# Performance work log

Hardware: AMD Instinct MI355X
Metric: run time of the kernel (lower is better)

## Reference

```python
import jax, jax.numpy as jnp
import numpy as np

B = 512
N_DRUGS = 4096
H_DRUG = 1023          # per-drug feature dim; input to MLP is 2*(H_DRUG+1) = 2048
N_CELL = 32
DIMS = [2048, 2048, 1024, 512, 1]


def setup_inputs() -> dict:
    key = jax.random.key(0)
    ks = jax.random.split(key, 12)
    pairs = jax.random.randint(ks[0], (B, 2), 0, N_DRUGS)
    cell_lines = jax.random.randint(ks[1], (B,), 0, N_CELL)
    attrs = jax.random.normal(ks[2], (B, 4), dtype=jnp.float32)
    h_drug = jax.random.normal(ks[3], (N_DRUGS, H_DRUG), dtype=jnp.float32)
    # shared Linear layers (torch Linear: y = x @ W.T + b), kaiming-uniform-ish init
    def lin(k, fan_in, fan_out):
        k1, k2 = jax.random.split(k)
        bound = 1.0 / np.sqrt(fan_in)
        W = jax.random.uniform(k1, (fan_out, fan_in), jnp.float32, -bound, bound)
        b = jax.random.uniform(k2, (fan_out,), jnp.float32, -bound, bound)
        return W, b
    W0, b0 = lin(ks[4], DIMS[0], DIMS[1])
    W1, b1 = lin(ks[5], DIMS[1], DIMS[2])
    # cell-line specific layers: 1/100 * randn
    L0 = 0.01 * jax.random.normal(ks[6], (N_CELL, DIMS[3], DIMS[2]), dtype=jnp.float32)
    O0 = 0.01 * jax.random.normal(ks[7], (N_CELL, DIMS[3], 1), dtype=jnp.float32)
    L1 = 0.01 * jax.random.normal(ks[8], (N_CELL, DIMS[4], DIMS[3]), dtype=jnp.float32)
    O1 = 0.01 * jax.random.normal(ks[9], (N_CELL, DIMS[4], 1), dtype=jnp.float32)
    return {"pairs": pairs, "cell_lines": cell_lines, "attrs": attrs, "h_drug": h_drug,
            "W0": W0, "b0": b0, "W1": W1, "b1": b1,
            "L0": L0, "O0": O0, "L1": L1, "O1": O1}


def reference(pairs, cell_lines, attrs, h_drug, W0, b0, W1, b1, L0, O0, L1, O1):
    n_attr = attrs.shape[1] // 2
    h1 = h_drug[pairs[:, 0]]                               # [B, H_DRUG]
    h2 = h_drug[pairs[:, 1]]
    bd1 = jnp.concatenate([h1, attrs[:, n_attr - 1:n_attr]], axis=1)
    bd2 = jnp.concatenate([h2, attrs[:, -1:]], axis=1)
    # original flips order with p=0.5 (data augmentation); fixed to (bd1, bd2) for determinism
    x = jnp.concatenate([bd1, bd2], axis=1)                # [B, 2048]
    # shared MLP (note: original applies relu(relu(x)) == relu(x))
    x = jax.nn.relu(x @ W0.T + b0)                         # [B, 2048]
    x = jax.nn.relu(x @ W1.T + b1)                         # [B, 1024]
    # cell-line-specific layers: gather per-sample weight and batched matvec
    x = jax.nn.relu(jnp.einsum('boi,bi->bo', L0[cell_lines], x) + O0[cell_lines, :, 0])  # [B, 512]
    x = jnp.einsum('boi,bi->bo', L1[cell_lines], x) + O1[cell_lines, :, 0]               # [B, 1]
    return x[:, 0]
```

## Files before the change

kernel.cpp:

```cpp
#include <hip/hip_runtime.h>

typedef short s16x8 __attribute__((ext_vector_type(8)));
typedef float f32x4 __attribute__((ext_vector_type(4)));
typedef unsigned short u16;

#define BATCH 512
#define HD    1023
#define K0    2048
#define N0    2048
#define N1    1024
#define N2    512

__device__ __forceinline__ u16 f2bf(float f) {
  unsigned u = __builtin_bit_cast(unsigned, f);
  unsigned r = (u + 0x7fffu + ((u >> 16) & 1u)) >> 16;
  return (u16)r;
}

__device__ __forceinline__ s16x8 pack8(f32x4 a, f32x4 b) {
  s16x8 r;
  r[0] = (short)f2bf(a[0]); r[1] = (short)f2bf(a[1]);
  r[2] = (short)f2bf(a[2]); r[3] = (short)f2bf(a[3]);
  r[4] = (short)f2bf(b[0]); r[5] = (short)f2bf(b[1]);
  r[6] = (short)f2bf(b[2]); r[7] = (short)f2bf(b[3]);
  return r;
}

__global__ __launch_bounds__(256) void k_gather(const int* __restrict__ pairs,
    const float* __restrict__ attrs, const float* __restrict__ h_drug,
    u16* __restrict__ xb) {
  int b = blockIdx.x;
  const float* h0 = h_drug + (size_t)pairs[2 * b] * HD;
  const float* h1 = h_drug + (size_t)pairs[2 * b + 1] * HD;
  u16* xr = xb + (size_t)b * K0;
  for (int i = threadIdx.x; i < HD; i += 256) {
    xr[i] = f2bf(h0[i]);
    xr[1024 + i] = f2bf(h1[i]);
  }
  if (threadIdx.x == 0) {
    xr[1023] = f2bf(attrs[4 * b + 1]);
    xr[2047] = f2bf(attrs[4 * b + 3]);
  }
}

#define GI(s, t) { \
  const size_t ab = (size_t)(t) * 128; const int wf = (t) * 64; \
  pa0_##s = *(const s16x8*)(agp0 + ab); \
  if constexpr (AF == 2) pa1_##s = *(const s16x8*)(agp1 + ab); \
  pw0_##s = *(const f32x4*)(wgp + wf); pw1_##s = *(const f32x4*)(wgp + wf + 4); }

#define GS(s, t, DOLOAD) { \
  char* buf = lds[(s) & 1]; \
  *(s16x8*)(buf + awo0) = pa0_##s; \
  if constexpr (AF == 2) *(s16x8*)(buf + awo1) = pa1_##s; \
  *(s16x8*)(buf + ABYTES + bwo0) = pack8(pw0_##s, pw1_##s); \
  asm volatile("s_waitcnt lgkmcnt(0)" ::: "memory"); \
  __builtin_amdgcn_s_barrier(); \
  asm volatile("" ::: "memory"); \
  if (DOLOAD) GI(s, (t) + 4) \
  __builtin_amdgcn_s_setprio(1); \
  _Pragma("unroll") \
  for (int ks = 0; ks < 2; ++ks) { \
    const int kq = ((ks << 6) | lk) ^ sw; \
    s16x8 a0 = *(const s16x8*)(buf + aoff + kq); \
    s16x8 b0 = *(const s16x8*)(buf + ABYTES + boff + kq); \
    acc0 = __builtin_amdgcn_mfma_f32_16x16x32_bf16(a0, b0, acc0, 0, 0, 0); \
    if constexpr (AF == 2) { \
      s16x8 a1 = *(const s16x8*)(buf + aoff + 2048 + kq); \
      acc1 = __builtin_amdgcn_mfma_f32_16x16x32_bf16(a1, b0, acc1, 0, 0, 0); \
    } \
  } \
  __builtin_amdgcn_s_setprio(0); }

template <int BM>
__global__ __launch_bounds__(256) void k_gemm(
    const u16* __restrict__ A, const float* __restrict__ W,
    const float* __restrict__ bias, u16* __restrict__ Y, int N) {
  constexpr int K = 2048;
  constexpr int AF = BM / 32;
  constexpr int ABYTES = BM * 128;
  constexpr int NBMSH = (BM == 64) ? 3 : 4;
  __shared__ char lds[2][ABYTES + 4096];
  const int tid = threadIdx.x;
  const int w = tid >> 6, l = tid & 63;
  const int wr = w >> 1, wc = w & 1;
  const int lrow = l & 15;
  const int lk = (l >> 4) << 4;
  const int sw = (lrow & 7) << 4;

  const int wgid = (blockIdx.x & 7) * 64 + (blockIdx.x >> 3);
  const int bn = wgid >> NBMSH, bm = wgid & ((1 << NBMSH) - 1);

  const size_t K2 = (size_t)K * 2;
  const char* Ag = (const char*)A + (size_t)bm * BM * K2;
  const float* Wg = W + (size_t)bn * 32 * K;

  const int o0 = tid * 16;
  const int ar0 = o0 >> 7, ac0 = o0 & 127;
  const char* agp0 = Ag + (size_t)ar0 * K2 + ac0;
  const int awo0 = (ar0 << 7) + (ac0 ^ ((ar0 & 7) << 4));
  const int o1 = o0 + 4096;
  const int ar1 = o1 >> 7, ac1 = o1 & 127;
  const char* agp1 = Ag + (size_t)ar1 * K2 + ac1;
  const int awo1 = (ar1 << 7) + (ac1 ^ ((ar1 & 7) << 4));

  const int br = tid >> 3, bq = tid & 7;
  const float* wgp = Wg + (size_t)br * K + bq * 8;
  const int bwo0 = (br << 7) + ((bq * 16) ^ ((br & 7) << 4));

  const int aoff = (wr * (BM / 2) + lrow) * 128;
  const int boff = (wc * 16 + lrow) * 128;

  f32x4 acc0 = {}, acc1 = {};
  s16x8 pa0_0, pa0_1, pa0_2, pa0_3;
  s16x8 pa1_0, pa1_1, pa1_2, pa1_3;
  f32x4 pw0_0, pw1_0, pw0_1, pw1_1, pw0_2, pw1_2, pw0_3, pw1_3;

  GI(0, 0) GI(1, 1) GI(2, 2) GI(3, 3)
  constexpr int NT = 32;
  int t = 0;
  for (; t < NT - 4; t += 4) {
    GS(0, t, 1) GS(1, t + 1, 1) GS(2, t + 2, 1) GS(3, t + 3, 1)
  }
  GS(0, t, 0) GS(1, t + 1, 0) GS(2, t + 2, 0) GS(3, t + 3, 0)

  const int colg = bn * 32 + wc * 16 + lrow;
  const int rowb = bm * BM + wr * (BM / 2) + ((l >> 4) << 2);
  const float bv = bias[colg];
#pragma unroll
  for (int fa = 0; fa < AF; ++fa)
#pragma unroll
    for (int r = 0; r < 4; ++r) {
      float v = (fa ? acc1 : acc0)[r] + bv;
      v = v > 0.f ? v : 0.f;
      Y[(size_t)(rowb + fa * 16 + r) * N + colg] = f2bf(v);
    }
}

#define H_ISSUE(S, ch) { \
  const float* src = hsrc + (ch) * 256; \
  q0_##S = *(const f32x4*)(src);      q1_##S = *(const f32x4*)(src + 4); \
  q2_##S = *(const f32x4*)(src + 8);  q3_##S = *(const f32x4*)(src + 12); \
  q4_##S = *(const f32x4*)(src + 16); q5_##S = *(const f32x4*)(src + 20); \
  q6_##S = *(const f32x4*)(src + 24); q7_##S = *(const f32x4*)(src + 28); }

#define H_WRITE(S, ch) { \
  char* dst = lbuf[(ch) & 1] + (hrow << 9); \
  *(s16x8*)(dst + ((hcb + 0)  ^ hswz)) = pack8(q0_##S, q1_##S); \
  *(s16x8*)(dst + ((hcb + 16) ^ hswz)) = pack8(q2_##S, q3_##S); \
  *(s16x8*)(dst + ((hcb + 32) ^ hswz)) = pack8(q4_##S, q5_##S); \
  *(s16x8*)(dst + ((hcb + 48) ^ hswz)) = pack8(q6_##S, q7_##S); }

#define H_SYNC { \
  asm volatile("s_waitcnt lgkmcnt(0)" ::: "memory"); \
  __builtin_amdgcn_s_barrier(); \
  asm volatile("" ::: "memory"); }

#define H_MFMA(ch) { \
  const char* bb = lbuf[(ch) & 1]; \
  s16x8 bv0 = *(const s16x8*)(bb + ((0 * 16 + lrow) << 9) + kboff); \
  s16x8 bv1 = *(const s16x8*)(bb + ((1 * 16 + lrow) << 9) + kboff); \
  s16x8 bv2 = *(const s16x8*)(bb + ((2 * 16 + lrow) << 9) + kboff); \
  s16x8 bv3 = *(const s16x8*)(bb + ((3 * 16 + lrow) << 9) + kboff); \
  s16x8 av0 = *(const s16x8*)(ap0 + (ch) * 256); \
  s16x8 av1 = *(const s16x8*)(ap1 + (ch) * 256); \
  __builtin_amdgcn_s_setprio(1); \
  acc[0][0] = __builtin_amdgcn_mfma_f32_16x16x32_bf16(av0, bv0, acc[0][0], 0, 0, 0); \
  acc[0][1] = __builtin_amdgcn_mfma_f32_16x16x32_bf16(av0, bv1, acc[0][1], 0, 0, 0); \
  acc[0][2] = __builtin_amdgcn_mfma_f32_16x16x32_bf16(av0, bv2, acc[0][2], 0, 0, 0); \
  acc[0][3] = __builtin_amdgcn_mfma_f32_16x16x32_bf16(av0, bv3, acc[0][3], 0, 0, 0); \
  acc[1][0] = __builtin_amdgcn_mfma_f32_16x16x32_bf16(av1, bv0, acc[1][0], 0, 0, 0); \
  acc[1][1] = __builtin_amdgcn_mfma_f32_16x16x32_bf16(av1, bv1, acc[1][1], 0, 0, 0); \
  acc[1][2] = __builtin_amdgcn_mfma_f32_16x16x32_bf16(av1, bv2, acc[1][2], 0, 0, 0); \
  acc[1][3] = __builtin_amdgcn_mfma_f32_16x16x32_bf16(av1, bv3, acc[1][3], 0, 0, 0); \
  __builtin_amdgcn_s_setprio(0); }

__global__ __launch_bounds__(512) void k_head(
    const int* __restrict__ cells, const u16* __restrict__ y2b,
    const float* __restrict__ L0, const float* __restrict__ O0,
    const float* __restrict__ L1, float* __restrict__ pp) {
  __shared__ int slist[544];
  __shared__ int scnt;
  __shared__ float red[8][2048];
  __shared__ char lbuf[2][32768];
  const int tid = threadIdx.x;
  const int c = blockIdx.x >> 3, rt = blockIdx.x & 7;
  if (tid == 0) scnt = 0;
  __syncthreads();
  for (int i = tid; i < BATCH; i += 512)
    if (cells[i] == c) slist[atomicAdd(&scnt, 1)] = i;
  __syncthreads();
  const int ns = scnt;
  if (ns == 0) return;
  const int npad = (ns + 31) & ~31;
  for (int i = ns + tid; i < npad; i += 512) slist[i] = slist[0];
  __syncthreads();

  const int w = tid >> 6, l = tid & 63;
  const int lrow = l & 15;
  const int r0 = rt * 64;
  const float* L0c = L0 + ((size_t)c * N2 + r0) * N1;
  const int hrow = tid >> 3;
  const int hcb = (tid & 7) * 64;
  const int hswz = (hrow & 7) << 4;
  const float* hsrc = L0c + (size_t)hrow * N1 + (tid & 7) * 32;
  const int kboff = ((w * 64 + ((l >> 4) << 4)) ^ ((lrow & 7) << 4));

  f32x4 q0_A, q1_A, q2_A, q3_A, q4_A, q5_A, q6_A, q7_A;
  f32x4 q0_B, q1_B, q2_B, q3_B, q4_B, q5_B, q6_B, q7_B;

  for (int cb = 0; cb < npad; cb += 32) {
    const u16* ap0 = y2b + (size_t)slist[cb + lrow] * N1 + w * 32 + ((l >> 4) << 3);
    const u16* ap1 = y2b + (size_t)slist[cb + 16 + lrow] * N1 + w * 32 + ((l >> 4) << 3);
    f32x4 acc[2][4] = {};
    H_ISSUE(A, 0)
    H_WRITE(A, 0)
    H_ISSUE(B, 1)
    H_SYNC
    H_MFMA(0)
    H_WRITE(B, 1)
    H_ISSUE(A, 2)
    H_SYNC
    H_MFMA(1)
    H_WRITE(A, 2)
    H_ISSUE(B, 3)
    H_SYNC
    H_MFMA(2)
    H_WRITE(B, 3)
    H_SYNC
    H_MFMA(3)

    __syncthreads();
#pragma unroll
    for (int h = 0; h < 2; ++h)
#pragma unroll
      for (int fb = 0; fb < 4; ++fb)
#pragma unroll
        for (int r = 0; r < 4; ++r) {
          const int s0 = h * 16 + (l >> 4) * 4 + r;
          red[w][s0 * 64 + fb * 16 + lrow] = acc[h][fb][r];
        }
    __syncthreads();
    {
      const int s = tid >> 4;
      const int rq = (tid & 15) * 4;
      if (cb + s < ns) {
        float p = 0.f;
#pragma unroll
        for (int j = 0; j < 4; ++j) {
          const int r = rq + j, e = s * 64 + r;
          float v = red[0][e] + red[1][e] + red[2][e] + red[3][e] +
                    red[4][e] + red[5][e] + red[6][e] + red[7][e] +
                    O0[(size_t)c * N2 + r0 + r];
          v = v > 0.f ? v : 0.f;
          p += v * L1[(size_t)c * N2 + r0 + r];
        }
#pragma unroll
        for (int off = 8; off; off >>= 1) p += __shfl_xor(p, off, 16);
        if ((tid & 15) == 0) pp[(size_t)rt * BATCH + slist[cb + s]] = p;
      }
    }
  }
}

__global__ __launch_bounds__(512) void k_final(
    const int* __restrict__ cells, const float* __restrict__ pp,
    const float* __restrict__ O1, float* __restrict__ out) {
  const int b = threadIdx.x;
  float s = O1[cells[b]];
#pragma unroll
  for (int rt = 0; rt < 8; ++rt) s += pp[(size_t)rt * BATCH + b];
  out[b] = s;
}

extern "C" void kernel_launch(void* const* d_in, const int* in_sizes, int n_in,
                              void* d_out, int out_size, void* d_ws, size_t ws_size,
                              hipStream_t stream) {
  const int*   pairs  = (const int*)d_in[0];
  const int*   cells  = (const int*)d_in[1];
  const float* attrs  = (const float*)d_in[2];
  const float* h_drug = (const float*)d_in[3];
  const float* W0     = (const float*)d_in[4];
  const float* b0     = (const float*)d_in[5];
  const float* W1     = (const float*)d_in[6];
  const float* b1     = (const float*)d_in[7];
  const float* L0     = (const float*)d_in[8];
  const float* O0     = (const float*)d_in[9];
  const float* L1     = (const float*)d_in[10];
  const float* O1     = (const float*)d_in[11];
  float* out = (float*)d_out;

  char* ws = (char*)d_ws;
  u16*   xb  = (u16*)(ws);
  u16*   y1b = (u16*)(ws + (2u << 20));
  u16*   y2b = (u16*)(ws + (4u << 20));
  float* pp  = (float*)(ws + (5u << 20));

  k_gather<<<BATCH, 256, 0, stream>>>(pairs, attrs, h_drug, xb);
  k_gemm<64><<<512, 256, 0, stream>>>(xb, W0, b0, y1b, N0);
  k_gemm<32><<<512, 256, 0, stream>>>(y1b, W1, b1, y2b, N1);
  k_head<<<256, 512, 0, stream>>>(cells, y2b, L0, O0, L1, pp);
  k_final<<<1, 512, 0, stream>>>(cells, pp, O1, out);
}
```

Measured before the change: 52.98 us.

## Split-K first GEMM with 64x64 tiles, fold final reduction into atomics

The first GEMM now uses 64x64 output tiles with a two-way split over K. It writes fp32 partials that a new reduction kernel sums with bias and ReLU before converting to bf16. This is meant to raise per-tile reuse of the fp32 weights while keeping 512 workgroups. The final tiny kernel is removed: the gather kernel seeds the output with O1 and the head kernel accumulates with atomicAdd. bf16 packing also moves to v_cvt_pk_bf16_f32 inline asm. The change adds 8 MB of partial traffic and an extra launch, and the atomics make the summation order nondeterministic.

Result: no change. 52.24 us (-1.4%).

```diff
diff --git a/kernel.cpp b/kernel.cpp
--- a/kernel.cpp
+++ b/kernel.cpp
@@ -18,17 +18,18 @@
 }
 
 __device__ __forceinline__ s16x8 pack8(f32x4 a, f32x4 b) {
-  s16x8 r;
-  r[0] = (short)f2bf(a[0]); r[1] = (short)f2bf(a[1]);
-  r[2] = (short)f2bf(a[2]); r[3] = (short)f2bf(a[3]);
-  r[4] = (short)f2bf(b[0]); r[5] = (short)f2bf(b[1]);
-  r[6] = (short)f2bf(b[2]); r[7] = (short)f2bf(b[3]);
-  return r;
+  union { unsigned u[4]; s16x8 v; } r;
+  asm("v_cvt_pk_bf16_f32 %0, %1, %2" : "=v"(r.u[0]) : "v"(a[0]), "v"(a[1]));
+  asm("v_cvt_pk_bf16_f32 %0, %1, %2" : "=v"(r.u[1]) : "v"(a[2]), "v"(a[3]));
+  asm("v_cvt_pk_bf16_f32 %0, %1, %2" : "=v"(r.u[2]) : "v"(b[0]), "v"(b[1]));
+  asm("v_cvt_pk_bf16_f32 %0, %1, %2" : "=v"(r.u[3]) : "v"(b[2]), "v"(b[3]));
+  return r.v;
 }
 
 __global__ __launch_bounds__(256) void k_gather(const int* __restrict__ pairs,
     const float* __restrict__ attrs, const float* __restrict__ h_drug,
-    u16* __restrict__ xb) {
+    u16* __restrict__ xb, const int* __restrict__ cells,
+    const float* __restrict__ O1, float* __restrict__ out) {
   int b = blockIdx.x;
   const float* h0 = h_drug + (size_t)pairs[2 * b] * HD;
   const float* h1 = h_drug + (size_t)pairs[2 * b + 1] * HD;
@@ -40,19 +41,139 @@
   if (threadIdx.x == 0) {
     xr[1023] = f2bf(attrs[4 * b + 1]);
     xr[2047] = f2bf(attrs[4 * b + 3]);
-  }
+    out[b] = O1[cells[b]];
+  }
+}
+
+#define GI1(s, t) { \
+  const size_t ab = (size_t)(t) * 128; const int wf = (t) * 64; \
+  pa0_##s = *(const s16x8*)(agp0 + ab); \
+  pa1_##s = *(const s16x8*)(agp1 + ab); \
+  pw0_##s = *(const f32x4*)(wgp + wf);     pw1_##s = *(const f32x4*)(wgp + wf + 4); \
+  pw2_##s = *(const f32x4*)(wgp + wf + 8); pw3_##s = *(const f32x4*)(wgp + wf + 12); }
+
+#define GS1(s, t, DOLOAD) { \
+  char* buf = lds[(s) & 1]; \
+  *(s16x8*)(buf + awo0) = pa0_##s; \
+  *(s16x8*)(buf + awo1) = pa1_##s; \
+  *(s16x8*)(buf + 8192 + bwo0) = pack8(pw0_##s, pw1_##s); \
+  *(s16x8*)(buf + 8192 + bwo1) = pack8(pw2_##s, pw3_##s); \
+  asm volatile("s_waitcnt lgkmcnt(0)" ::: "memory"); \
+  __builtin_amdgcn_s_barrier(); \
+  asm volatile("" ::: "memory"); \
+  if (DOLOAD) GI1(s, (t) + 4) \
+  __builtin_amdgcn_s_setprio(1); \
+  _Pragma("unroll") \
+  for (int ks = 0; ks < 2; ++ks) { \
+    const int kq = ((ks << 6) | lk) ^ sw; \
+    s16x8 a0 = *(const s16x8*)(buf + aoff + kq); \
+    s16x8 a1 = *(const s16x8*)(buf + aoff + 2048 + kq); \
+    s16x8 b0 = *(const s16x8*)(buf + 8192 + boff + kq); \
+    s16x8 b1 = *(const s16x8*)(buf + 8192 + boff + 2048 + kq); \
+    acc00 = __builtin_amdgcn_mfma_f32_16x16x32_bf16(a0, b0, acc00, 0, 0, 0); \
+    acc01 = __builtin_amdgcn_mfma_f32_16x16x32_bf16(a0, b1, acc01, 0, 0, 0); \
+    acc10 = __builtin_amdgcn_mfma_f32_16x16x32_bf16(a1, b0, acc10, 0, 0, 0); \
+    acc11 = __builtin_amdgcn_mfma_f32_16x16x32_bf16(a1, b1, acc11, 0, 0, 0); \
+  } \
+  __builtin_amdgcn_s_setprio(0); }
+
+__global__ __launch_bounds__(256) void k_gemm1(
+    const u16* __restrict__ A, const float* __restrict__ W,
+    float* __restrict__ P) {
+  constexpr int K = 2048, N = 2048;
+  __shared__ char lds[2][16384];
+  const int tid = threadIdx.x;
+  const int w = tid >> 6, l = tid & 63;
+  const int wr = w >> 1, wc = w & 1;
+  const int lrow = l & 15;
+  const int lk = (l >> 4) << 4;
+  const int sw = (lrow & 7) << 4;
+
+  const int wgid = (blockIdx.x & 7) * 64 + (blockIdx.x >> 3);
+  const int bn = wgid >> 4;
+  const int bm = (wgid >> 1) & 7;
+  const int sub = wgid & 1;
+
+  const size_t K2 = (size_t)K * 2;
+  const char* Ag = (const char*)A + (size_t)bm * 64 * K2 + (size_t)sub * 2048;
+  const float* Wg = W + (size_t)bn * 64 * K + sub * 1024;
+
+  const int o0 = tid * 16;
+  const int ar0 = o0 >> 7, ac0 = o0 & 127;
+  const char* agp0 = Ag + (size_t)ar0 * K2 + ac0;
+  const int awo0 = (ar0 << 7) + (ac0 ^ ((ar0 & 7) << 4));
+  const int o1 = o0 + 4096;
+  const int ar1 = o1 >> 7, ac1 = o1 & 127;
+  const char* agp1 = Ag + (size_t)ar1 * K2 + ac1;
+  const int awo1 = (ar1 << 7) + (ac1 ^ ((ar1 & 7) << 4));
+
+  const int br = tid >> 2, bq = tid & 3;
+  const float* wgp = Wg + (size_t)br * K + bq * 16;
+  const int bsw = (br & 7) << 4;
+  const int bwo0 = (br << 7) + ((bq * 32) ^ bsw);
+  const int bwo1 = (br << 7) + ((bq * 32 + 16) ^ bsw);
+
+  const int aoff = (wr * 32 + lrow) * 128;
+  const int boff = (wc * 32 + lrow) * 128;
+
+  f32x4 acc00 = {}, acc01 = {}, acc10 = {}, acc11 = {};
+  s16x8 pa0_0, pa0_1, pa0_2, pa0_3;
+  s16x8 pa1_0, pa1_1, pa1_2, pa1_3;
+  f32x4 pw0_0, pw1_0, pw2_0, pw3_0;
+  f32x4 pw0_1, pw1_1, pw2_1, pw3_1;
+  f32x4 pw0_2, pw1_2, pw2_2, pw3_2;
+  f32x4 pw0_3, pw1_3, pw2_3, pw3_3;
+
+  GI1(0, 0) GI1(1, 1) GI1(2, 2) GI1(3, 3)
+  constexpr int NT = 16;
+  int t = 0;
+  for (; t < NT - 4; t += 4) {
+    GS1(0, t, 1) GS1(1, t + 1, 1) GS1(2, t + 2, 1) GS1(3, t + 3, 1)
+  }
+  GS1(0, t, 0) GS1(1, t + 1, 0) GS1(2, t + 2, 0) GS1(3, t + 3, 0)
+
+  float* Pp = P + (size_t)sub * (BATCH * (size_t)N);
+  const int colg = bn * 64 + wc * 32 + lrow;
+  const int rowg = bm * 64 + wr * 32 + ((l >> 4) << 2);
+#pragma unroll
+  for (int r = 0; r < 4; ++r) {
+    Pp[(size_t)(rowg + r) * N + colg]           = acc00[r];
+    Pp[(size_t)(rowg + r) * N + colg + 16]      = acc01[r];
+    Pp[(size_t)(rowg + 16 + r) * N + colg]      = acc10[r];
+    Pp[(size_t)(rowg + 16 + r) * N + colg + 16] = acc11[r];
+  }
+}
+
+__global__ __launch_bounds__(256) void k_red1(
+    const float* __restrict__ P, const float* __restrict__ bias,
+    u16* __restrict__ Y) {
+  const int i = blockIdx.x * 256 + threadIdx.x;
+  const size_t e = (size_t)i * 8;
+  const int col = (int)(e & 2047);
+  f32x4 a0 = *(const f32x4*)(P + e);
+  f32x4 a1 = *(const f32x4*)(P + e + 4);
+  f32x4 c0 = *(const f32x4*)(P + (size_t)BATCH * N0 + e);
+  f32x4 c1 = *(const f32x4*)(P + (size_t)BATCH * N0 + e + 4);
+  f32x4 d0 = *(const f32x4*)(bias + col);
+  f32x4 d1 = *(const f32x4*)(bias + col + 4);
+#pragma unroll
+  for (int j = 0; j < 4; ++j) {
+    float v0 = a0[j] + c0[j] + d0[j];
+    float v1 = a1[j] + c1[j] + d1[j];
+    a0[j] = v0 > 0.f ? v0 : 0.f;
+    a1[j] = v1 > 0.f ? v1 : 0.f;
+  }
+  *(s16x8*)(Y + e) = pack8(a0, a1);
 }
 
 #define GI(s, t) { \
   const size_t ab = (size_t)(t) * 128; const int wf = (t) * 64; \
   pa0_##s = *(const s16x8*)(agp0 + ab); \
-  if constexpr (AF == 2) pa1_##s = *(const s16x8*)(agp1 + ab); \
   pw0_##s = *(const f32x4*)(wgp + wf); pw1_##s = *(const f32x4*)(wgp + wf + 4); }
 
 #define GS(s, t, DOLOAD) { \
   char* buf = lds[(s) & 1]; \
   *(s16x8*)(buf + awo0) = pa0_##s; \
-  if constexpr (AF == 2) *(s16x8*)(buf + awo1) = pa1_##s; \
   *(s16x8*)(buf + ABYTES + bwo0) = pack8(pw0_##s, pw1_##s); \
   asm volatile("s_waitcnt lgkmcnt(0)" ::: "memory"); \
   __builtin_amdgcn_s_barrier(); \
@@ -65,21 +186,14 @@
     s16x8 a0 = *(const s16x8*)(buf + aoff + kq); \
     s16x8 b0 = *(const s16x8*)(buf + ABYTES + boff + kq); \
     acc0 = __builtin_amdgcn_mfma_f32_16x16x32_bf16(a0, b0, acc0, 0, 0, 0); \
-    if constexpr (AF == 2) { \
-      s16x8 a1 = *(const s16x8*)(buf + aoff + 2048 + kq); \
-      acc1 = __builtin_amdgcn_mfma_f32_16x16x32_bf16(a1, b0, acc1, 0, 0, 0); \
-    } \
   } \
   __builtin_amdgcn_s_setprio(0); }
 
-template <int BM>
-__global__ __launch_bounds__(256) void k_gemm(
+__global__ __launch_bounds__(256) void k_gemm2(
     const u16* __restrict__ A, const float* __restrict__ W,
-    const float* __restrict__ bias, u16* __restrict__ Y, int N) {
-  constexpr int K = 2048;
-  constexpr int AF = BM / 32;
-  constexpr int ABYTES = BM * 128;
-  constexpr int NBMSH = (BM == 64) ? 3 : 4;
+    const float* __restrict__ bias, u16* __restrict__ Y) {
+  constexpr int K = 2048, N = 1024;
+  constexpr int ABYTES = 32 * 128;
   __shared__ char lds[2][ABYTES + 4096];
   const int tid = threadIdx.x;
   const int w = tid >> 6, l = tid & 63;
@@ -89,31 +203,26 @@
   const int sw = (lrow & 7) << 4;
 
   const int wgid = (blockIdx.x & 7) * 64 + (blockIdx.x >> 3);
-  const int bn = wgid >> NBMSH, bm = wgid & ((1 << NBMSH) - 1);
+  const int bn = wgid >> 4, bm = wgid & 15;
 
   const size_t K2 = (size_t)K * 2;
-  const char* Ag = (const char*)A + (size_t)bm * BM * K2;
+  const char* Ag = (const char*)A + (size_t)bm * 32 * K2;
   const float* Wg = W + (size_t)bn * 32 * K;
 
   const int o0 = tid * 16;
   const int ar0 = o0 >> 7, ac0 = o0 & 127;
   const char* agp0 = Ag + (size_t)ar0 * K2 + ac0;
   const int awo0 = (ar0 << 7) + (ac0 ^ ((ar0 & 7) << 4));
-  const int o1 = o0 + 4096;
-  const int ar1 = o1 >> 7, ac1 = o1 & 127;
-  const char* agp1 = Ag + (size_t)ar1 * K2 + ac1;
-  const int awo1 = (ar1 << 7) + (ac1 ^ ((ar1 & 7) << 4));
 
   const int br = tid >> 3, bq = tid & 7;
   const float* wgp = Wg + (size_t)br * K + bq * 8;
   const int bwo0 = (br << 7) + ((bq * 16) ^ ((br & 7) << 4));
 
-  const int aoff = (wr * (BM / 2) + lrow) * 128;
+  const int aoff = (wr * 16 + lrow) * 128;
   const int boff = (wc * 16 + lrow) * 128;
 
-  f32x4 acc0 = {}, acc1 = {};
+  f32x4 acc0 = {};
   s16x8 pa0_0, pa0_1, pa0_2, pa0_3;
-  s16x8 pa1_0, pa1_1, pa1_2, pa1_3;
   f32x4 pw0_0, pw1_0, pw0_1, pw1_1, pw0_2, pw1_2, pw0_3, pw1_3;
 
   GI(0, 0) GI(1, 1) GI(2, 2) GI(3, 3)
@@ -125,16 +234,14 @@
   GS(0, t, 0) GS(1, t + 1, 0) GS(2, t + 2, 0) GS(3, t + 3, 0)
 
   const int colg = bn * 32 + wc * 16 + lrow;
-  const int rowb = bm * BM + wr * (BM / 2) + ((l >> 4) << 2);
+  const int rowb = bm * 32 + wr * 16 + ((l >> 4) << 2);
   const float bv = bias[colg];
 #pragma unroll
-  for (int fa = 0; fa < AF; ++fa)
-#pragma unroll
-    for (int r = 0; r < 4; ++r) {
-      float v = (fa ? acc1 : acc0)[r] + bv;
-      v = v > 0.f ? v : 0.f;
-      Y[(size_t)(rowb + fa * 16 + r) * N + colg] = f2bf(v);
-    }
+  for (int r = 0; r < 4; ++r) {
+    float v = acc0[r] + bv;
+    v = v > 0.f ? v : 0.f;
+    Y[(size_t)(rowb + r) * N + colg] = f2bf(v);
+  }
 }
 
 #define H_ISSUE(S, ch) { \
@@ -178,7 +285,7 @@
 __global__ __launch_bounds__(512) void k_head(
     const int* __restrict__ cells, const u16* __restrict__ y2b,
     const float* __restrict__ L0, const float* __restrict__ O0,
-    const float* __restrict__ L1, float* __restrict__ pp) {
+    const float* __restrict__ L1, float* __restrict__ out) {
   __shared__ int slist[544];
   __shared__ int scnt;
   __shared__ float red[8][2048];
@@ -257,20 +364,10 @@
         }
 #pragma unroll
         for (int off = 8; off; off >>= 1) p += __shfl_xor(p, off, 16);
-        if ((tid & 15) == 0) pp[(size_t)rt * BATCH + slist[cb + s]] = p;
+        if ((tid & 15) == 0) atomicAdd(&out[slist[cb + s]], p);
       }
     }
   }
-}
-
-__global__ __launch_bounds__(512) void k_final(
-    const int* __restrict__ cells, const float* __restrict__ pp,
-    const float* __restrict__ O1, float* __restrict__ out) {
-  const int b = threadIdx.x;
-  float s = O1[cells[b]];
-#pragma unroll
-  for (int rt = 0; rt < 8; ++rt) s += pp[(size_t)rt * BATCH + b];
-  out[b] = s;
 }
 
 extern "C" void kernel_launch(void* const* d_in, const int* in_sizes, int n_in,
@@ -294,11 +391,11 @@
   u16*   xb  = (u16*)(ws);
   u16*   y1b = (u16*)(ws + (2u << 20));
   u16*   y2b = (u16*)(ws + (4u << 20));
-  float* pp  = (float*)(ws + (5u << 20));
-
-  k_gather<<<BATCH, 256, 0, stream>>>(pairs, attrs, h_drug, xb);
-  k_gemm<64><<<512, 256, 0, stream>>>(xb, W0, b0, y1b, N0);
-  k_gemm<32><<<512, 256, 0, stream>>>(y1b, W1, b1, y2b, N1);
-  k_head<<<256, 512, 0, stream>>>(cells, y2b, L0, O0, L1, pp);
-  k_final<<<1, 512, 0, stream>>>(cells, pp, O1, out);
-}
+  float* P   = (float*)(ws + (5u << 20));
+
+  k_gather<<<BATCH, 256, 0, stream>>>(pairs, attrs, h_drug, xb, cells, O1, out);
+  k_gemm1<<<512, 256, 0, stream>>>(xb, W0, P);
+  k_red1<<<512, 256, 0, stream>>>(P, b0, y1b);
+  k_gemm2<<<512, 256, 0, stream>>>(y1b, W1, b1, y2b);
+  k_head<<<256, 512, 0, stream>>>(cells, y2b, L0, O0, L1, out);
+}
```

## Fuse drug gather into first GEMM and fold final reduction into head atomics

Applied to the files above, without the earlier changes.

The gather/convert kernel is removed: the first GEMM now loads fp32 drug features directly by pair index, appends the attribute column, and converts to bf16 while staging into LDS. The final reduction kernel is removed by having the second GEMM initialize the output with the O1 bias and the head kernel atomically add its partial sums. pack8 now uses the hardware packed bf16 convert instruction. Together these drop two launches and an intermediate round trip, at the cost of unaligned fp32 A loads and float atomics whose order is nondeterministic.

Measured after the change: 54.92 us. +3.7%, slower.

```diff
diff --git a/kernel.cpp b/kernel.cpp
--- a/kernel.cpp
+++ b/kernel.cpp
@@ -18,42 +18,128 @@
 }
 
 __device__ __forceinline__ s16x8 pack8(f32x4 a, f32x4 b) {
-  s16x8 r;
-  r[0] = (short)f2bf(a[0]); r[1] = (short)f2bf(a[1]);
-  r[2] = (short)f2bf(a[2]); r[3] = (short)f2bf(a[3]);
-  r[4] = (short)f2bf(b[0]); r[5] = (short)f2bf(b[1]);
-  r[6] = (short)f2bf(b[2]); r[7] = (short)f2bf(b[3]);
-  return r;
-}
-
-__global__ __launch_bounds__(256) void k_gather(const int* __restrict__ pairs,
-    const float* __restrict__ attrs, const float* __restrict__ h_drug,
-    u16* __restrict__ xb) {
-  int b = blockIdx.x;
-  const float* h0 = h_drug + (size_t)pairs[2 * b] * HD;
-  const float* h1 = h_drug + (size_t)pairs[2 * b + 1] * HD;
-  u16* xr = xb + (size_t)b * K0;
-  for (int i = threadIdx.x; i < HD; i += 256) {
-    xr[i] = f2bf(h0[i]);
-    xr[1024 + i] = f2bf(h1[i]);
+  union { unsigned u[4]; s16x8 v; } r;
+  asm("v_cvt_pk_bf16_f32 %0, %1, %2" : "=v"(r.u[0]) : "v"(a[0]), "v"(a[1]));
+  asm("v_cvt_pk_bf16_f32 %0, %1, %2" : "=v"(r.u[1]) : "v"(a[2]), "v"(a[3]));
+  asm("v_cvt_pk_bf16_f32 %0, %1, %2" : "=v"(r.u[2]) : "v"(b[0]), "v"(b[1]));
+  asm("v_cvt_pk_bf16_f32 %0, %1, %2" : "=v"(r.u[3]) : "v"(b[2]), "v"(b[3]));
+  return r.v;
+}
+
+__device__ __forceinline__ f32x4 ld4u(const float* p) {
+  f32x4 v; __builtin_memcpy(&v, p, 16); return v;
+}
+
+
+#define LDA(dx, dy, bh0, bh1, att0, att1, t) { \
+  const float* bp = ((t) < 16) ? (bh0) : (bh1); \
+  const int off = (((t) & 15) << 6) + ac; \
+  dx = ld4u(bp + off); \
+  if ((((t) & 15) == 15) && (ac == 56)) { \
+    dy[0] = bp[off + 4]; dy[1] = bp[off + 5]; dy[2] = bp[off + 6]; \
+    dy[3] = ((t) < 16) ? (att0) : (att1); \
+  } else { \
+    dy = ld4u(bp + off + 4); \
+  } }
+
+#define GIA(s, t) { \
+  LDA(pax0_##s, pay0_##s, a0h0, a0h1, at00, at01, t) \
+  LDA(pax1_##s, pay1_##s, a1h0, a1h1, at10, at11, t) \
+  pw0_##s = *(const f32x4*)(wgp + (t) * 64); \
+  pw1_##s = *(const f32x4*)(wgp + (t) * 64 + 4); }
+
+#define GSA(s, t, DOLOAD) { \
+  char* buf = lds[(s) & 1]; \
+  *(s16x8*)(buf + awo0) = pack8(pax0_##s, pay0_##s); \
+  *(s16x8*)(buf + awo1) = pack8(pax1_##s, pay1_##s); \
+  *(s16x8*)(buf + 8192 + bwo0) = pack8(pw0_##s, pw1_##s); \
+  asm volatile("s_waitcnt lgkmcnt(0)" ::: "memory"); \
+  __builtin_amdgcn_s_barrier(); \
+  asm volatile("" ::: "memory"); \
+  if (DOLOAD) GIA(s, (t) + 4) \
+  __builtin_amdgcn_s_setprio(1); \
+  _Pragma("unroll") \
+  for (int ks = 0; ks < 2; ++ks) { \
+    const int kq = ((ks << 6) | lk) ^ sw; \
+    s16x8 a0 = *(const s16x8*)(buf + aoff + kq); \
+    s16x8 a1 = *(const s16x8*)(buf + aoff + 2048 + kq); \
+    s16x8 b0 = *(const s16x8*)(buf + 8192 + boff + kq); \
+    acc0 = __builtin_amdgcn_mfma_f32_16x16x32_bf16(a0, b0, acc0, 0, 0, 0); \
+    acc1 = __builtin_amdgcn_mfma_f32_16x16x32_bf16(a1, b0, acc1, 0, 0, 0); \
+  } \
+  __builtin_amdgcn_s_setprio(0); }
+
+__global__ __launch_bounds__(256) void k_fgemm1(
+    const int* __restrict__ pairs, const float* __restrict__ attrs,
+    const float* __restrict__ h_drug, const float* __restrict__ W,
+    const float* __restrict__ bias, u16* __restrict__ Y) {
+  constexpr int K = 2048, N = 2048;
+  __shared__ char lds[2][8192 + 4096];
+  const int tid = threadIdx.x;
+  const int w = tid >> 6, l = tid & 63;
+  const int wr = w >> 1, wc = w & 1;
+  const int lrow = l & 15;
+  const int lk = (l >> 4) << 4;
+  const int sw = (lrow & 7) << 4;
+
+  const int wgid = (blockIdx.x & 7) * 64 + (blockIdx.x >> 3);
+  const int bn = wgid >> 3, bm = wgid & 7;
+
+  const int arow = tid >> 3;
+  const int ac = (tid & 7) * 8;
+  const int s0 = bm * 64 + arow, s1 = s0 + 32;
+  const float* a0h0 = h_drug + (size_t)pairs[2 * s0] * HD;
+  const float* a0h1 = h_drug + (size_t)pairs[2 * s0 + 1] * HD;
+  const float* a1h0 = h_drug + (size_t)pairs[2 * s1] * HD;
+  const float* a1h1 = h_drug + (size_t)pairs[2 * s1 + 1] * HD;
+  const float at00 = attrs[4 * s0 + 1], at01 = attrs[4 * s0 + 3];
+  const float at10 = attrs[4 * s1 + 1], at11 = attrs[4 * s1 + 3];
+  const int awo0 = (arow << 7) + ((ac * 2) ^ ((arow & 7) << 4));
+  const int awo1 = awo0 + (32 << 7);
+
+  const int br = tid >> 3, bq = tid & 7;
+  const float* wgp = W + (size_t)(bn * 32 + br) * K + bq * 8;
+  const int bwo0 = (br << 7) + ((bq * 16) ^ ((br & 7) << 4));
+
+  const int aoff = (wr * 32 + lrow) * 128;
+  const int boff = (wc * 16 + lrow) * 128;
+
+  f32x4 acc0 = {}, acc1 = {};
+  f32x4 pax0_0, pay0_0, pax1_0, pay1_0, pw0_0, pw1_0;
+  f32x4 pax0_1, pay0_1, pax1_1, pay1_1, pw0_1, pw1_1;
+  f32x4 pax0_2, pay0_2, pax1_2, pay1_2, pw0_2, pw1_2;
+  f32x4 pax0_3, pay0_3, pax1_3, pay1_3, pw0_3, pw1_3;
+
+  GIA(0, 0) GIA(1, 1) GIA(2, 2) GIA(3, 3)
+  constexpr int NT = 32;
+  int t = 0;
+  for (; t < NT - 4; t += 4) {
+    GSA(0, t, 1) GSA(1, t + 1, 1) GSA(2, t + 2, 1) GSA(3, t + 3, 1)
   }
-  if (threadIdx.x == 0) {
-    xr[1023] = f2bf(attrs[4 * b + 1]);
-    xr[2047] = f2bf(attrs[4 * b + 3]);
-  }
+  GSA(0, t, 0) GSA(1, t + 1, 0) GSA(2, t + 2, 0) GSA(3, t + 3, 0)
+
+  const int colg = bn * 32 + wc * 16 + lrow;
+  const int rowb = bm * 64 + wr * 32 + ((l >> 4) << 2);
+  const float bv = bias[colg];
+#pragma unroll
+  for (int fa = 0; fa < 2; ++fa)
+#pragma unroll
+    for (int r = 0; r < 4; ++r) {
+      float v = (fa ? acc1 : acc0)[r] + bv;
+      v = v > 0.f ? v : 0.f;
+      Y[(size_t)(rowb + fa * 16 + r) * N + colg] = f2bf(v);
+    }
 }
 
 #define GI(s, t) { \
   const size_t ab = (size_t)(t) * 128; const int wf = (t) * 64; \
   pa0_##s = *(const s16x8*)(agp0 + ab); \
-  if constexpr (AF == 2) pa1_##s = *(const s16x8*)(agp1 + ab); \
   pw0_##s = *(const f32x4*)(wgp + wf); pw1_##s = *(const f32x4*)(wgp + wf + 4); }
 
 #define GS(s, t, DOLOAD) { \
   char* buf = lds[(s) & 1]; \
+  *(s16x8*)(buf + ABYTES + bwo0) = pack8(pw0_##s, pw1_##s); \
   *(s16x8*)(buf + awo0) = pa0_##s; \
-  if constexpr (AF == 2) *(s16x8*)(buf + awo1) = pa1_##s; \
-  *(s16x8*)(buf + ABYTES + bwo0) = pack8(pw0_##s, pw1_##s); \
   asm volatile("s_waitcnt lgkmcnt(0)" ::: "memory"); \
   __builtin_amdgcn_s_barrier(); \
   asm volatile("" ::: "memory"); \
@@ -65,23 +151,21 @@
     s16x8 a0 = *(const s16x8*)(buf + aoff + kq); \
     s16x8 b0 = *(const s16x8*)(buf + ABYTES + boff + kq); \
     acc0 = __builtin_amdgcn_mfma_f32_16x16x32_bf16(a0, b0, acc0, 0, 0, 0); \
-    if constexpr (AF == 2) { \
-      s16x8 a1 = *(const s16x8*)(buf + aoff + 2048 + kq); \
-      acc1 = __builtin_amdgcn_mfma_f32_16x16x32_bf16(a1, b0, acc1, 0, 0, 0); \
-    } \
   } \
   __builtin_amdgcn_s_setprio(0); }
 
-template <int BM>
-__global__ __launch_bounds__(256) void k_gemm(
+__global__ __launch_bounds__(256) void k_gemm2(
     const u16* __restrict__ A, const float* __restrict__ W,
-    const float* __restrict__ bias, u16* __restrict__ Y, int N) {
-  constexpr int K = 2048;
-  constexpr int AF = BM / 32;
-  constexpr int ABYTES = BM * 128;
-  constexpr int NBMSH = (BM == 64) ? 3 : 4;
+    const float* __restrict__ bias, u16* __restrict__ Y,
+    const int* __restrict__ cells, const float* __restrict__ O1,
+    float* __restrict__ out) {
+  constexpr int K = 2048, N = 1024;
+  constexpr int ABYTES = 32 * 128;
   __shared__ char lds[2][ABYTES + 4096];
   const int tid = threadIdx.x;
+
+  if (blockIdx.x < 2) out[blockIdx.x * 256 + tid] = O1[cells[blockIdx.x * 256 + tid]];
+
   const int w = tid >> 6, l = tid & 63;
   const int wr = w >> 1, wc = w & 1;
   const int lrow = l & 15;
@@ -89,31 +173,26 @@
   const int sw = (lrow & 7) << 4;
 
   const int wgid = (blockIdx.x & 7) * 64 + (blockIdx.x >> 3);
-  const int bn = wgid >> NBMSH, bm = wgid & ((1 << NBMSH) - 1);
+  const int bn = wgid >> 4, bm = wgid & 15;
 
   const size_t K2 = (size_t)K * 2;
-  const char* Ag = (const char*)A + (size_t)bm * BM * K2;
+  const char* Ag = (const char*)A + (size_t)bm * 32 * K2;
   const float* Wg = W + (size_t)bn * 32 * K;
 
   const int o0 = tid * 16;
   const int ar0 = o0 >> 7, ac0 = o0 & 127;
   const char* agp0 = Ag + (size_t)ar0 * K2 + ac0;
   const int awo0 = (ar0 << 7) + (ac0 ^ ((ar0 & 7) << 4));
-  const int o1 = o0 + 4096;
-  const int ar1 = o1 >> 7, ac1 = o1 & 127;
-  const char* agp1 = Ag + (size_t)ar1 * K2 + ac1;
-  const int awo1 = (ar1 << 7) + (ac1 ^ ((ar1 & 7) << 4));
 
   const int br = tid >> 3, bq = tid & 7;
   const float* wgp = Wg + (size_t)br * K + bq * 8;
   const int bwo0 = (br << 7) + ((bq * 16) ^ ((br & 7) << 4));
 
-  const int aoff = (wr * (BM / 2) + lrow) * 128;
+  const int aoff = (wr * 16 + lrow) * 128;
   const int boff = (wc * 16 + lrow) * 128;
 
-  f32x4 acc0 = {}, acc1 = {};
+  f32x4 acc0 = {};
   s16x8 pa0_0, pa0_1, pa0_2, pa0_3;
-  s16x8 pa1_0, pa1_1, pa1_2, pa1_3;
   f32x4 pw0_0, pw1_0, pw0_1, pw1_1, pw0_2, pw1_2, pw0_3, pw1_3;
 
   GI(0, 0) GI(1, 1) GI(2, 2) GI(3, 3)
@@ -125,16 +204,14 @@
   GS(0, t, 0) GS(1, t + 1, 0) GS(2, t + 2, 0) GS(3, t + 3, 0)
 
   const int colg = bn * 32 + wc * 16 + lrow;
-  const int rowb = bm * BM + wr * (BM / 2) + ((l >> 4) << 2);
+  const int rowb = bm * 32 + wr * 16 + ((l >> 4) << 2);
   const float bv = bias[colg];
 #pragma unroll
-  for (int fa = 0; fa < AF; ++fa)
-#pragma unroll
-    for (int r = 0; r < 4; ++r) {
-      float v = (fa ? acc1 : acc0)[r] + bv;
-      v = v > 0.f ? v : 0.f;
-      Y[(size_t)(rowb + fa * 16 + r) * N + colg] = f2bf(v);
-    }
+  for (int r = 0; r < 4; ++r) {
+    float v = acc0[r] + bv;
+    v = v > 0.f ? v : 0.f;
+    Y[(size_t)(rowb + r) * N + colg] = f2bf(v);
+  }
 }
 
 #define H_ISSUE(S, ch) { \
@@ -178,7 +255,7 @@
 __global__ __launch_bounds__(512) void k_head(
     const int* __restrict__ cells, const u16* __restrict__ y2b,
     const float* __restrict__ L0, const float* __restrict__ O0,
-    const float* __restrict__ L1, float* __restrict__ pp) {
+    const float* __restrict__ L1, float* __restrict__ out) {
   __shared__ int slist[544];
   __shared__ int scnt;
   __shared__ float red[8][2048];
@@ -257,20 +334,10 @@
         }
 #pragma unroll
         for (int off = 8; off; off >>= 1) p += __shfl_xor(p, off, 16);
-        if ((tid & 15) == 0) pp[(size_t)rt * BATCH + slist[cb + s]] = p;
+        if ((tid & 15) == 0) atomicAdd(&out[slist[cb + s]], p);
       }
     }
   }
-}
-
-__global__ __launch_bounds__(512) void k_final(
-    const int* __restrict__ cells, const float* __restrict__ pp,
-    const float* __restrict__ O1, float* __restrict__ out) {
-  const int b = threadIdx.x;
-  float s = O1[cells[b]];
-#pragma unroll
-  for (int rt = 0; rt < 8; ++rt) s += pp[(size_t)rt * BATCH + b];
-  out[b] = s;
 }
 
 extern "C" void kernel_launch(void* const* d_in, const int* in_sizes, int n_in,
@@ -291,14 +358,10 @@
   float* out = (float*)d_out;
 
   char* ws = (char*)d_ws;
-  u16*   xb  = (u16*)(ws);
-  u16*   y1b = (u16*)(ws + (2u << 20));
-  u16*   y2b = (u16*)(ws + (4u << 20));
-  float* pp  = (float*)(ws + (5u << 20));
-
-  k_gather<<<BATCH, 256, 0, stream>>>(pairs, attrs, h_drug, xb);
-  k_gemm<64><<<512, 256, 0, stream>>>(xb, W0, b0, y1b, N0);
-  k_gemm<32><<<512, 256, 0, stream>>>(y1b, W1, b1, y2b, N1);
-  k_head<<<256, 512, 0, stream>>>(cells, y2b, L0, O0, L1, pp);
-  k_final<<<1, 512, 0, stream>>>(cells, pp, O1, out);
-}
+  u16* y1b = (u16*)(ws);
+  u16* y2b = (u16*)(ws + (2u << 20));
+
+  k_fgemm1<<<512, 256, 0, stream>>>(pairs, attrs, h_drug, W0, b0, y1b);
+  k_gemm2<<<512, 256, 0, stream>>>(y1b, W1, b1, y2b, cells, O1, out);
+  k_head<<<256, 512, 0, stream>>>(cells, y2b, L0, O0, L1, out);
+}
```

## Pre-convert weights to bf16 in fused prep kernel, drop final reduction kernel

Applied to the files above, without the earlier changes.

Merges the gather with a pass that converts W0 and W1 to bf16 in workspace, so the GEMMs load bf16 B tiles like A tiles instead of fp32 loads plus in-loop packing. The final reduction kernel is removed: prep writes the O1 bias into out and the head kernel accumulates partial sums with atomicAdd. Weight packing now uses the hardware packed bf16 convert instruction. This trades one extra read/write pass over the weights each call for less GEMM load bandwidth, less per-tile conversion work and one fewer launch, at the cost of nondeterministic float atomic summation order.

After: 48.26 us. 8.9% less time.

```diff
diff --git a/kernel.cpp b/kernel.cpp
--- a/kernel.cpp
+++ b/kernel.cpp
@@ -18,42 +18,60 @@
 }
 
 __device__ __forceinline__ s16x8 pack8(f32x4 a, f32x4 b) {
-  s16x8 r;
-  r[0] = (short)f2bf(a[0]); r[1] = (short)f2bf(a[1]);
-  r[2] = (short)f2bf(a[2]); r[3] = (short)f2bf(a[3]);
-  r[4] = (short)f2bf(b[0]); r[5] = (short)f2bf(b[1]);
-  r[6] = (short)f2bf(b[2]); r[7] = (short)f2bf(b[3]);
-  return r;
-}
-
-__global__ __launch_bounds__(256) void k_gather(const int* __restrict__ pairs,
-    const float* __restrict__ attrs, const float* __restrict__ h_drug,
-    u16* __restrict__ xb) {
-  int b = blockIdx.x;
-  const float* h0 = h_drug + (size_t)pairs[2 * b] * HD;
-  const float* h1 = h_drug + (size_t)pairs[2 * b + 1] * HD;
-  u16* xr = xb + (size_t)b * K0;
-  for (int i = threadIdx.x; i < HD; i += 256) {
-    xr[i] = f2bf(h0[i]);
-    xr[1024 + i] = f2bf(h1[i]);
+  union { unsigned u[4]; s16x8 v; } r;
+  asm("v_cvt_pk_bf16_f32 %0, %1, %2" : "=v"(r.u[0]) : "v"(a[0]), "v"(a[1]));
+  asm("v_cvt_pk_bf16_f32 %0, %1, %2" : "=v"(r.u[1]) : "v"(a[2]), "v"(a[3]));
+  asm("v_cvt_pk_bf16_f32 %0, %1, %2" : "=v"(r.u[2]) : "v"(b[0]), "v"(b[1]));
+  asm("v_cvt_pk_bf16_f32 %0, %1, %2" : "=v"(r.u[3]) : "v"(b[2]), "v"(b[3]));
+  return r.v;
+}
+
+__global__ __launch_bounds__(256) void k_prep(
+    const int* __restrict__ pairs, const float* __restrict__ attrs,
+    const float* __restrict__ h_drug, const float* __restrict__ W0,
+    const float* __restrict__ W1, const int* __restrict__ cells,
+    const float* __restrict__ O1, u16* __restrict__ xb,
+    u16* __restrict__ w0b, u16* __restrict__ w1b, float* __restrict__ out) {
+  const int bid = blockIdx.x, tid = threadIdx.x;
+  if (bid < 512) {
+    const int b = bid;
+    const float* h0 = h_drug + (size_t)pairs[2 * b] * HD;
+    const float* h1 = h_drug + (size_t)pairs[2 * b + 1] * HD;
+    u16* xr = xb + (size_t)b * K0;
+    for (int i = tid; i < HD; i += 256) {
+      xr[i] = f2bf(h0[i]);
+      xr[1024 + i] = f2bf(h1[i]);
+    }
+    if (tid == 0) {
+      xr[1023] = f2bf(attrs[4 * b + 1]);
+      xr[2047] = f2bf(attrs[4 * b + 3]);
+      out[b] = O1[cells[b]];
+    }
+  } else if (bid < 1536) {
+    const size_t e = ((size_t)(bid - 512) * 256 + tid) * 16;
+    f32x4 a = *(const f32x4*)(W0 + e),     b2 = *(const f32x4*)(W0 + e + 4);
+    f32x4 c = *(const f32x4*)(W0 + e + 8), d  = *(const f32x4*)(W0 + e + 12);
+    *(s16x8*)(w0b + e)     = pack8(a, b2);
+    *(s16x8*)(w0b + e + 8) = pack8(c, d);
+  } else {
+    const size_t e = ((size_t)(bid - 1536) * 256 + tid) * 16;
+    f32x4 a = *(const f32x4*)(W1 + e),     b2 = *(const f32x4*)(W1 + e + 4);
+    f32x4 c = *(const f32x4*)(W1 + e + 8), d  = *(const f32x4*)(W1 + e + 12);
+    *(s16x8*)(w1b + e)     = pack8(a, b2);
+    *(s16x8*)(w1b + e + 8) = pack8(c, d);
   }
-  if (threadIdx.x == 0) {
-    xr[1023] = f2bf(attrs[4 * b + 1]);
-    xr[2047] = f2bf(attrs[4 * b + 3]);
-  }
 }
 
 #define GI(s, t) { \
-  const size_t ab = (size_t)(t) * 128; const int wf = (t) * 64; \
-  pa0_##s = *(const s16x8*)(agp0 + ab); \
-  if constexpr (AF == 2) pa1_##s = *(const s16x8*)(agp1 + ab); \
-  pw0_##s = *(const f32x4*)(wgp + wf); pw1_##s = *(const f32x4*)(wgp + wf + 4); }
+  pa0_##s = *(const s16x8*)(agp0 + (size_t)(t) * 128); \
+  if constexpr (AF == 2) pa1_##s = *(const s16x8*)(agp1 + (size_t)(t) * 128); \
+  pb_##s = *(const s16x8*)(bgp0 + (size_t)(t) * 128); }
 
 #define GS(s, t, DOLOAD) { \
   char* buf = lds[(s) & 1]; \
   *(s16x8*)(buf + awo0) = pa0_##s; \
   if constexpr (AF == 2) *(s16x8*)(buf + awo1) = pa1_##s; \
-  *(s16x8*)(buf + ABYTES + bwo0) = pack8(pw0_##s, pw1_##s); \
+  *(s16x8*)(buf + ABYTES + bwo0) = pb_##s; \
   asm volatile("s_waitcnt lgkmcnt(0)" ::: "memory"); \
   __builtin_amdgcn_s_barrier(); \
   asm volatile("" ::: "memory"); \
@@ -72,10 +90,10 @@
   } \
   __builtin_amdgcn_s_setprio(0); }
 
-template <int BM>
+template <int BM, int N>
 __global__ __launch_bounds__(256) void k_gemm(
-    const u16* __restrict__ A, const float* __restrict__ W,
-    const float* __restrict__ bias, u16* __restrict__ Y, int N) {
+    const u16* __restrict__ A, const u16* __restrict__ B,
+    const float* __restrict__ bias, u16* __restrict__ Y) {
   constexpr int K = 2048;
   constexpr int AF = BM / 32;
   constexpr int ABYTES = BM * 128;
@@ -93,7 +111,7 @@
 
   const size_t K2 = (size_t)K * 2;
   const char* Ag = (const char*)A + (size_t)bm * BM * K2;
-  const float* Wg = W + (size_t)bn * 32 * K;
+  const char* Bg = (const char*)B + (size_t)(bn * 32) * K2;
 
   const int o0 = tid * 16;
   const int ar0 = o0 >> 7, ac0 = o0 & 127;
@@ -104,9 +122,8 @@
   const char* agp1 = Ag + (size_t)ar1 * K2 + ac1;
   const int awo1 = (ar1 << 7) + (ac1 ^ ((ar1 & 7) << 4));
 
-  const int br = tid >> 3, bq = tid & 7;
-  const float* wgp = Wg + (size_t)br * K + bq * 8;
-  const int bwo0 = (br << 7) + ((bq * 16) ^ ((br & 7) << 4));
+  const char* bgp0 = Bg + (size_t)ar0 * K2 + ac0;
+  const int bwo0 = awo0;
 
   const int aoff = (wr * (BM / 2) + lrow) * 128;
   const int boff = (wc * 16 + lrow) * 128;
@@ -114,7 +131,7 @@
   f32x4 acc0 = {}, acc1 = {};
   s16x8 pa0_0, pa0_1, pa0_2, pa0_3;
   s16x8 pa1_0, pa1_1, pa1_2, pa1_3;
-  f32x4 pw0_0, pw1_0, pw0_1, pw1_1, pw0_2, pw1_2, pw0_3, pw1_3;
+  s16x8 pb_0, pb_1, pb_2, pb_3;
 
   GI(0, 0) GI(1, 1) GI(2, 2) GI(3, 3)
   constexpr int NT = 32;
@@ -178,7 +195,7 @@
 __global__ __launch_bounds__(512) void k_head(
     const int* __restrict__ cells, const u16* __restrict__ y2b,
     const float* __restrict__ L0, const float* __restrict__ O0,
-    const float* __restrict__ L1, float* __restrict__ pp) {
+    const float* __restrict__ L1, float* __restrict__ out) {
   __shared__ int slist[544];
   __shared__ int scnt;
   __shared__ float red[8][2048];
@@ -257,20 +274,10 @@
         }
 #pragma unroll
         for (int off = 8; off; off >>= 1) p += __shfl_xor(p, off, 16);
-        if ((tid & 15) == 0) pp[(size_t)rt * BATCH + slist[cb + s]] = p;
+        if ((tid & 15) == 0) atomicAdd(&out[slist[cb + s]], p);
       }
     }
   }
-}
-
-__global__ __launch_bounds__(512) void k_final(
-    const int* __restrict__ cells, const float* __restrict__ pp,
-    const float* __restrict__ O1, float* __restrict__ out) {
-  const int b = threadIdx.x;
-  float s = O1[cells[b]];
-#pragma unroll
-  for (int rt = 0; rt < 8; ++rt) s += pp[(size_t)rt * BATCH + b];
-  out[b] = s;
 }
 
 extern "C" void kernel_launch(void* const* d_in, const int* in_sizes, int n_in,
@@ -291,14 +298,15 @@
   float* out = (float*)d_out;
 
   char* ws = (char*)d_ws;
-  u16*   xb  = (u16*)(ws);
-  u16*   y1b = (u16*)(ws + (2u << 20));
-  u16*   y2b = (u16*)(ws + (4u << 20));
-  float* pp  = (float*)(ws + (5u << 20));
-
-  k_gather<<<BATCH, 256, 0, stream>>>(pairs, attrs, h_drug, xb);
-  k_gemm<64><<<512, 256, 0, stream>>>(xb, W0, b0, y1b, N0);
-  k_gemm<32><<<512, 256, 0, stream>>>(y1b, W1, b1, y2b, N1);
-  k_head<<<256, 512, 0, stream>>>(cells, y2b, L0, O0, L1, pp);
-  k_final<<<1, 512, 0, stream>>>(cells, pp, O1, out);
-}
+  u16* xb  = (u16*)(ws);
+  u16* w0b = (u16*)(ws + (2u  << 20));
+  u16* w1b = (u16*)(ws + (10u << 20));
+  u16* y1b = (u16*)(ws + (14u << 20));
+  u16* y2b = (u16*)(ws + (16u << 20));
+
+  k_prep<<<2048, 256, 0, stream>>>(pairs, attrs, h_drug, W0, W1, cells, O1,
+                                   xb, w0b, w1b, out);
+  k_gemm<64, N0><<<512, 256, 0, stream>>>(xb, w0b, b0, y1b);
+  k_gemm<32, N1><<<512, 256, 0, stream>>>(y1b, w1b, b1, y2b);
+  k_head<<<256, 512, 0, stream>>>(cells, y2b, L0, O0, L1, out);
+}
```
